# Optimization experiments

Hardware: AMD Instinct MI355X
Metric: run time of the kernel (lower is better)

## Reference

```python
import jax, jax.numpy as jnp
import numpy as np

B, T, H = 1, 2048, 2048
HEADS, DH = 16, 128  # head_dim = H // HEADS
K = 50               # block size
NEG = -1e9


def setup_inputs() -> dict:
    key = jax.random.key(0)
    ks = jax.random.split(key, 6)
    x = jax.random.normal(ks[0], (B, T, H), jnp.float32)
    mask = jnp.ones((B, T), jnp.float32)
    bias = jax.random.normal(ks[1], (B, HEADS, T, T), jnp.float32) * 0.02
    s = 1.0 / np.sqrt(H)
    Wq = jax.random.normal(ks[2], (H, HEADS, DH), jnp.float32) * s
    Wk = jax.random.normal(ks[3], (H, HEADS, DH), jnp.float32) * s
    Wv = jax.random.normal(ks[4], (H, HEADS, DH), jnp.float32) * s
    Wo = jax.random.normal(ks[5], (HEADS, DH, H), jnp.float32) * (1.0 / np.sqrt(H))
    return {"x_BxTxH": x, "mask_BxT": mask, "attention_bias_BxHxTxT": bias,
            "Wq": Wq, "Wk": Wk, "Wv": Wv, "Wo": Wo}


def _local_self_attention(x, mask, bias, Wq, Wk, Wv, Wo):
    b, t, h = x.shape
    extra = K - t % K          # module always pads (pads a full block if t % K == 0)
    p = t + extra
    n = p // K
    # pad + block the inputs: [b, n, K, h]
    xb = jnp.pad(x, ((0, 0), (0, extra), (0, 0))).reshape(b, n, K, h)
    # pad mask with -1e9 (as in the module), block, build pairwise mask via multiply
    mb = jnp.pad(mask, ((0, 0), (0, extra)), constant_values=NEG).reshape(b, n, K)
    pair = mb[..., :, None] * mb[..., None, :]              # [b, n, K, K]
    mask_bias = jnp.where(pair > 0, 0.0, NEG)[:, :, None]   # [b, n, 1, K, K] (broadcast heads)
    # pad attention bias and extract block-diagonal: [b, n, heads, K, K]
    bp = jnp.pad(bias, ((0, 0), (0, 0), (0, extra), (0, extra)))
    nb = bp.reshape(b, HEADS, n, K, n, K)
    idx = jnp.arange(n)
    blk_bias = nb[:, :, idx, :, idx, :]          # [n, b, heads, K, K]
    blk_bias = jnp.transpose(blk_bias, (1, 0, 2, 3, 4))  # [b, n, heads, K, K]
    # per-block multi-head attention (no qkv bias, query scaled by head_dim**-0.5)
    q = jnp.einsum('bnkh,hef->bnkef', xb, Wq) * (DH ** -0.5)
    k = jnp.einsum('bnkh,hef->bnkef', xb, Wk)
    v = jnp.einsum('bnkh,hef->bnkef', xb, Wv)
    logits = jnp.einsum('bnqef,bnkef->bneqk', q, k) + blk_bias + mask_bias
    attn = jax.nn.softmax(logits, axis=-1)
    out = jnp.einsum('bneqk,bnkef->bnqef', attn, v)
    out = jnp.einsum('bnqef,efh->bnqh', out, Wo).reshape(b, p, h)
    return out[:, :t, :]


def reference(x_BxTxH, mask_BxT, attention_bias_BxHxTxT, Wq, Wk, Wv, Wo):
    return _local_self_attention(x_BxTxH, mask_BxT, attention_bias_BxHxTxT, Wq, Wk, Wv, Wo)
```

## Files before the change

### kernel.cpp

```cpp
#include <hip/hip_runtime.h>
#include <hip/hip_bf16.h>

typedef _Float16 f16x8 __attribute__((ext_vector_type(8)));
typedef float f32x4 __attribute__((ext_vector_type(4)));

#define T_DIM 2048
#define H_DIM 2048
#define N_HEADS 16
#define DH 128
#define KBLK 50
#define NBLK 41
#define NEGV (-1.0e9f)
#define QSCALE 0.08838834764831845f

__device__ __forceinline__ void gl_lds16(const void* g, void* l) {
    __builtin_amdgcn_global_load_lds(
        (const __attribute__((address_space(1))) void*)g,
        (__attribute__((address_space(3))) void*)l, 16, 0, 0);
}

__global__ __launch_bounds__(256) void prep_kernel(const float* __restrict__ x,
                                                   const float* __restrict__ Wq,
                                                   const float* __restrict__ Wk,
                                                   const float* __restrict__ Wv,
                                                   const float* __restrict__ Wo,
                                                   _Float16* __restrict__ xb,
                                                   _Float16* __restrict__ WT,
                                                   _Float16* __restrict__ WoT) {
    __shared__ float tile[32][33];
    int z = blockIdx.z;
    int tx = threadIdx.x, ty = threadIdx.y;
    if (z == 4) {
        if (blockIdx.y >= 32) return;
        int flat = blockIdx.y * 64 + blockIdx.x;
        int i = (flat * 256 + ty * 32 + tx) * 8;
        float4 a = *(const float4*)&x[i];
        float4 b = *(const float4*)&x[i + 4];
        f16x8 o = {(_Float16)a.x, (_Float16)a.y, (_Float16)a.z, (_Float16)a.w,
                   (_Float16)b.x, (_Float16)b.y, (_Float16)b.z, (_Float16)b.w};
        *(f16x8*)&xb[i] = o;
        return;
    }
    const float* src = (z == 0) ? Wq : (z == 1) ? Wk : (z == 2) ? Wv : Wo;
    _Float16* dst = (z == 3) ? WoT : (WT + (size_t)z * T_DIM * H_DIM);
    int bx = blockIdx.x * 32, by = blockIdx.y * 32;
#pragma unroll
    for (int i = 0; i < 4; i++)
        tile[ty + i * 8][tx] = src[(size_t)(by + ty + i * 8) * H_DIM + bx + tx];
    __syncthreads();
#pragma unroll
    for (int i = 0; i < 4; i++)
        dst[(size_t)(bx + ty + i * 8) * H_DIM + by + tx] = (_Float16)tile[tx][ty + i * 8];
}

__global__ __launch_bounds__(512, 2) void qkv192_kernel(const _Float16* __restrict__ A,
                                                        const _Float16* __restrict__ BT,
                                                        _Float16* __restrict__ qkv) {
    const int K = 2048, NT = 32;
    __shared__ _Float16 smem[57344];
    _Float16* sA0 = smem;
    _Float16* sA1 = smem + 16384;
    _Float16* sB0 = smem + 32768;
    _Float16* sB1 = smem + 45056;

    int tid = threadIdx.x;
    int lane = tid & 63, wave = tid >> 6;
    int wm = wave >> 2, wn = wave & 3;
    int cb = lane & 15, hi = lane >> 4;

    int bid = blockIdx.x;
    int swz = (bid & 7) * 32 + (bid >> 3);
    int by = swz >> 5, bx = swz & 31;
    int bm = by * 256, bn = bx * 192;

    f32x4 acc[8][3];
#pragma unroll
    for (int m = 0; m < 8; m++)
#pragma unroll
        for (int n = 0; n < 3; n++) acc[m][n] = (f32x4){0.f, 0.f, 0.f, 0.f};

    int rp = tid >> 3, cc = tid & 7;
    int scol = ((cc ^ (rp & 7)) << 3);

    auto stageA = [&](int t, int u) {
        int buf = t & 1;
        gl_lds16(A + (size_t)(bm + u * 64 + rp) * K + (t << 6) + scol,
                 (buf ? sA1 : sA0) + u * 4096 + tid * 8);
    };
    auto stageB = [&](int t, int u) {
        int buf = t & 1;
        gl_lds16(BT + (size_t)(bn + u * 64 + rp) * K + (t << 6) + scol,
                 (buf ? sB1 : sB0) + u * 4096 + tid * 8);
    };

    f16x8 a_lo[4][2], a_hi[4][2], b01[2][2], b2[2];

    stageA(0, 0); stageA(0, 1); stageA(0, 2); stageA(0, 3);
    stageB(0, 0); stageB(0, 1); stageB(0, 2);
    stageA(1, 0); stageA(1, 1); stageA(1, 2); stageA(1, 3);
    asm volatile("s_waitcnt vmcnt(4)" ::: "memory");
    __builtin_amdgcn_s_barrier();

    for (int t = 0; t < NT; t++) {
        int buf = t & 1;
        const char* bA = (const char*)(buf ? sA1 : sA0);
        const char* bB = (const char*)(buf ? sB1 : sB0);
#pragma unroll
        for (int mf = 0; mf < 4; mf++) {
            int ra = wm * 128 + mf * 16 + cb;
#pragma unroll
            for (int ks = 0; ks < 2; ks++)
                a_lo[mf][ks] = *(const f16x8*)(bA + (ra << 7) +
                                               ((ks * 64 + hi * 16) ^ ((ra & 7) << 4)));
        }
#pragma unroll
        for (int nf = 0; nf < 2; nf++) {
            int rb = wn * 48 + nf * 16 + cb;
#pragma unroll
            for (int ks = 0; ks < 2; ks++)
                b01[nf][ks] = *(const f16x8*)(bB + (rb << 7) +
                                              ((ks * 64 + hi * 16) ^ ((rb & 7) << 4)));
        }
        if (t + 1 < NT) { stageB(t + 1, 0); stageB(t + 1, 1); }
        __builtin_amdgcn_s_barrier();
        asm volatile("s_waitcnt lgkmcnt(0)" ::: "memory");
        __builtin_amdgcn_s_setprio(1);
#pragma unroll
        for (int mf = 0; mf < 4; mf++)
#pragma unroll
            for (int nf = 0; nf < 2; nf++)
#pragma unroll
                for (int ks = 0; ks < 2; ks++)
                    acc[mf][nf] = __builtin_amdgcn_mfma_f32_16x16x32_f16(a_lo[mf][ks], b01[nf][ks], acc[mf][nf], 0, 0, 0);
        __builtin_amdgcn_s_setprio(0);
        __builtin_amdgcn_s_barrier();

#pragma unroll
        for (int mf = 0; mf < 4; mf++) {
            int ra = wm * 128 + 64 + mf * 16 + cb;
#pragma unroll
            for (int ks = 0; ks < 2; ks++)
                a_hi[mf][ks] = *(const f16x8*)(bA + (ra << 7) +
                                               ((ks * 64 + hi * 16) ^ ((ra & 7) << 4)));
        }
        {
            int rb = wn * 48 + 32 + cb;
#pragma unroll
            for (int ks = 0; ks < 2; ks++)
                b2[ks] = *(const f16x8*)(bB + (rb << 7) +
                                         ((ks * 64 + hi * 16) ^ ((rb & 7) << 4)));
        }
        if (t + 1 < NT) stageB(t + 1, 2);
        __builtin_amdgcn_s_barrier();
        asm volatile("s_waitcnt lgkmcnt(0)" ::: "memory");
        __builtin_amdgcn_s_setprio(1);
#pragma unroll
        for (int mf = 0; mf < 4; mf++)
#pragma unroll
            for (int ks = 0; ks < 2; ks++)
                acc[4 + mf][2] = __builtin_amdgcn_mfma_f32_16x16x32_f16(a_hi[mf][ks], b2[ks], acc[4 + mf][2], 0, 0, 0);
        __builtin_amdgcn_s_setprio(0);
        __builtin_amdgcn_s_barrier();

        if (t + 2 < NT) { stageA(t + 2, 0); stageA(t + 2, 1); }
        __builtin_amdgcn_s_barrier();
        __builtin_amdgcn_s_setprio(1);
#pragma unroll
        for (int mf = 0; mf < 4; mf++)
#pragma unroll
            for (int ks = 0; ks < 2; ks++)
                acc[mf][2] = __builtin_amdgcn_mfma_f32_16x16x32_f16(a_lo[mf][ks], b2[ks], acc[mf][2], 0, 0, 0);
        __builtin_amdgcn_s_setprio(0);
        __builtin_amdgcn_s_barrier();

        if (t + 2 < NT) { stageA(t + 2, 2); stageA(t + 2, 3); }
        if (t < NT - 2)
            asm volatile("s_waitcnt vmcnt(4)" ::: "memory");
        else if (t == NT - 2)
            asm volatile("s_waitcnt vmcnt(0)" ::: "memory");
        __builtin_amdgcn_s_barrier();
        __builtin_amdgcn_s_setprio(1);
#pragma unroll
        for (int mf = 0; mf < 4; mf++)
#pragma unroll
            for (int nf = 0; nf < 2; nf++)
#pragma unroll
                for (int ks = 0; ks < 2; ks++)
                    acc[4 + mf][nf] = __builtin_amdgcn_mfma_f32_16x16x32_f16(a_hi[mf][ks], b01[nf][ks], acc[4 + mf][nf], 0, 0, 0);
        __builtin_amdgcn_s_setprio(0);
        __builtin_amdgcn_s_barrier();
    }

#pragma unroll
    for (int p = 0; p < 2; p++) {
        if (p) __builtin_amdgcn_s_barrier();
        if (wm == p) {
#pragma unroll
            for (int mf = 0; mf < 8; mf++)
#pragma unroll
                for (int nf = 0; nf < 3; nf++) {
                    int col = wn * 48 + nf * 16 + cb;
                    float sc = ((bn + col) >> 11) == 0 ? QSCALE : 1.0f;
#pragma unroll
                    for (int r = 0; r < 4; r++) {
                        int row = mf * 16 + hi * 4 + r;
                        smem[row * 200 + col] = (_Float16)(acc[mf][nf][r] * sc);
                    }
                }
        }
        __builtin_amdgcn_s_barrier();
#pragma unroll
        for (int it = 0; it < 6; it++) {
            int c = it * 512 + tid;
            int row = c / 24, col8 = c - row * 24;
            int gm = bm + p * 128 + row;
            int gn = bn + col8 * 8;
            int tensor = gn >> 11;
            int ef = gn & 2047;
            int e = ef >> 7, f0 = ef & 127;
            uint4 v = *(const uint4*)&smem[row * 200 + col8 * 8];
            *(uint4*)(qkv + (size_t)tensor * (T_DIM * H_DIM) + (size_t)e * (T_DIM * DH) +
                      (size_t)gm * DH + f0) = v;
        }
    }
}

__global__ __launch_bounds__(512, 2) void oproj_kernel(const _Float16* __restrict__ A,
                                                       const _Float16* __restrict__ BT,
                                                       _Float16* __restrict__ part) {
    const int K = 2048, NT = 8;
    __shared__ _Float16 smem[65536];
    _Float16* sA0 = smem;
    _Float16* sA1 = smem + 16384;
    _Float16* sB0 = smem + 32768;
    _Float16* sB1 = smem + 49152;

    int tid = threadIdx.x;
    int lane = tid & 63, wave = tid >> 6;
    int wm = wave >> 2, wn = wave & 3;
    int cb = lane & 15, hi = lane >> 4;

    int bid = blockIdx.x;
    int s = bid & 3, tile = bid >> 2;
    int by = tile >> 3, bx = tile & 7;
    int bm = by * 256, bn = bx * 256;
    int kbase = s * 512;

    f32x4 acc[8][4];
#pragma unroll
    for (int m = 0; m < 8; m++)
#pragma unroll
        for (int n = 0; n < 4; n++) acc[m][n] = (f32x4){0.f, 0.f, 0.f, 0.f};

    auto stageP = [&](int t, int p) {
        int buf = t & 1, k0 = kbase + (t << 6);
        const _Float16* src = (p < 2) ? A + (size_t)(bm + ((p & 1) << 7)) * K + k0
                                      : BT + (size_t)(bn + ((p & 1) << 7)) * K + k0;
        _Float16* dst = ((p < 2) ? (buf ? sA1 : sA0) : (buf ? sB1 : sB0)) + ((p & 1) << 13);
#pragma unroll
        for (int l = 0; l < 2; l++) {
            int c = l * 512 + tid;
            int rp = c >> 3, cc = c & 7;
            int col = (cc ^ (rp & 7)) << 3;
            gl_lds16(src + (size_t)rp * K + col, dst + c * 8);
        }
    };

    f16x8 a_lo[4][2], a_hi[4][2], b_lo[2][2], b_hi[2][2];

    stageP(0, 0); stageP(0, 1); stageP(0, 2); stageP(0, 3);
    stageP(1, 0); stageP(1, 1);
    asm volatile("s_waitcnt vmcnt(4)" ::: "memory");
    __builtin_amdgcn_s_barrier();

    for (int t = 0; t < NT; t++) {
        int buf = t & 1;
        const char* bA = (const char*)(buf ? sA1 : sA0);
        const char* bB = (const char*)(buf ? sB1 : sB0);
#pragma unroll
        for (int m = 0; m < 4; m++) {
            int ra = wm * 128 + m * 16 + cb;
#pragma unroll
            for (int ks = 0; ks < 2; ks++)
                a_lo[m][ks] = *(const f16x8*)(bA + (ra << 7) +
                                              ((ks * 64 + hi * 16) ^ ((ra & 7) << 4)));
        }
#pragma unroll
        for (int n = 0; n < 2; n++) {
            int rb = wn * 64 + n * 16 + cb;
#pragma unroll
            for (int ks = 0; ks < 2; ks++)
                b_lo[n][ks] = *(const f16x8*)(bB + (rb << 7) +
                                              ((ks * 64 + hi * 16) ^ ((rb & 7) << 4)));
        }
        if (t + 1 < NT) stageP(t + 1, 2);
        __builtin_amdgcn_s_barrier();
        asm volatile("s_waitcnt lgkmcnt(0)" ::: "memory");
        __builtin_amdgcn_s_setprio(1);
#pragma unroll
        for (int m = 0; m < 4; m++)
#pragma unroll
            for (int n = 0; n < 2; n++)
#pragma unroll
                for (int ks = 0; ks < 2; ks++)
                    acc[m][n] = __builtin_amdgcn_mfma_f32_16x16x32_f16(a_lo[m][ks], b_lo[n][ks], acc[m][n], 0, 0, 0);
        __builtin_amdgcn_s_setprio(0);
        __builtin_amdgcn_s_barrier();

#pragma unroll
        for (int m = 0; m < 4; m++) {
            int ra = wm * 128 + 64 + m * 16 + cb;
#pragma unroll
            for (int ks = 0; ks < 2; ks++)
                a_hi[m][ks] = *(const f16x8*)(bA + (ra << 7) +
                                              ((ks * 64 + hi * 16) ^ ((ra & 7) << 4)));
        }
#pragma unroll
        for (int n = 0; n < 2; n++) {
            int rb = wn * 64 + 32 + n * 16 + cb;
#pragma unroll
            for (int ks = 0; ks < 2; ks++)
                b_hi[n][ks] = *(const f16x8*)(bB + (rb << 7) +
                                              ((ks * 64 + hi * 16) ^ ((rb & 7) << 4)));
        }
        if (t + 1 < NT) stageP(t + 1, 3);
        __builtin_amdgcn_s_barrier();
        asm volatile("s_waitcnt lgkmcnt(0)" ::: "memory");
        __builtin_amdgcn_s_setprio(1);
#pragma unroll
        for (int m = 0; m < 4; m++)
#pragma unroll
            for (int n = 0; n < 2; n++)
#pragma unroll
                for (int ks = 0; ks < 2; ks++)
                    acc[4 + m][2 + n] = __builtin_amdgcn_mfma_f32_16x16x32_f16(a_hi[m][ks], b_hi[n][ks], acc[4 + m][2 + n], 0, 0, 0);
        __builtin_amdgcn_s_setprio(0);
        __builtin_amdgcn_s_barrier();

        if (t + 2 < NT) stageP(t + 2, 0);
        __builtin_amdgcn_s_barrier();
        __builtin_amdgcn_s_setprio(1);
#pragma unroll
        for (int m = 0; m < 4; m++)
#pragma unroll
            for (int n = 0; n < 2; n++)
#pragma unroll
                for (int ks = 0; ks < 2; ks++)
                    acc[m][2 + n] = __builtin_amdgcn_mfma_f32_16x16x32_f16(a_lo[m][ks], b_hi[n][ks], acc[m][2 + n], 0, 0, 0);
        __builtin_amdgcn_s_setprio(0);
        __builtin_amdgcn_s_barrier();

        if (t + 2 < NT) stageP(t + 2, 1);
        if (t < NT - 2)
            asm volatile("s_waitcnt vmcnt(4)" ::: "memory");
        else if (t == NT - 2)
            asm volatile("s_waitcnt vmcnt(0)" ::: "memory");
        __builtin_amdgcn_s_barrier();
        __builtin_amdgcn_s_setprio(1);
#pragma unroll
        for (int m = 0; m < 4; m++)
#pragma unroll
            for (int n = 0; n < 2; n++)
#pragma unroll
                for (int ks = 0; ks < 2; ks++)
                    acc[4 + m][n] = __builtin_amdgcn_mfma_f32_16x16x32_f16(a_hi[m][ks], b_lo[n][ks], acc[4 + m][n], 0, 0, 0);
        __builtin_amdgcn_s_setprio(0);
        __builtin_amdgcn_s_barrier();
    }

    _Float16* pb = part + (size_t)s * T_DIM * H_DIM;
#pragma unroll
    for (int p = 0; p < 2; p++) {
        if (p) __builtin_amdgcn_s_barrier();
        if (wm == p) {
#pragma unroll
            for (int m = 0; m < 8; m++)
#pragma unroll
                for (int n = 0; n < 4; n++) {
                    int col = wn * 64 + ((n & 1) * 16) + ((n >> 1) * 32) + cb;
#pragma unroll
                    for (int r = 0; r < 4; r++) {
                        int row = ((m & 3) * 16) + ((m >> 2) * 64) + hi * 4 + r;
                        smem[row * 264 + col] = (_Float16)acc[m][n][r];
                    }
                }
        }
        __builtin_amdgcn_s_barrier();
#pragma unroll
        for (int it = 0; it < 8; it++) {
            int c = it * 512 + tid;
            int row = c >> 5, col8 = c & 31;
            int gm = bm + p * 128 + row;
            int gn = bn + col8 * 8;
            uint4 v = *(const uint4*)&smem[row * 264 + col8 * 8];
            *(uint4*)&pb[(size_t)gm * H_DIM + gn] = v;
        }
    }
}

__global__ __launch_bounds__(256) void reduce4_kernel(const _Float16* __restrict__ part,
                                                      float* __restrict__ out) {
    const size_t S = (size_t)T_DIM * H_DIM;
    int i = (blockIdx.x * 256 + threadIdx.x) * 8;
    f16x8 p0 = *(const f16x8*)&part[i];
    f16x8 p1 = *(const f16x8*)&part[S + i];
    f16x8 p2 = *(const f16x8*)&part[2 * S + i];
    f16x8 p3 = *(const f16x8*)&part[3 * S + i];
#pragma unroll
    for (int j = 0; j < 8; j++)
        out[i + j] = (float)p0[j] + (float)p1[j] + (float)p2[j] + (float)p3[j];
}

__global__ __launch_bounds__(256) void attn_kernel(const _Float16* __restrict__ qkvb,
                                                   const float* __restrict__ bias,
                                                   const float* __restrict__ mask,
                                                   _Float16* __restrict__ aout) {
    int bid = blockIdx.x;
    int n = bid >> 4, e = bid & 15;
    int t0 = n * KBLK;
    int valid = (T_DIM - t0 < KBLK) ? (T_DIM - t0) : KBLK;

    __shared__ _Float16 Qs[64 * 136];
    __shared__ _Float16 Ks[64 * 136];
    __shared__ _Float16 VTs[128 * 72];
    __shared__ _Float16 Ps[64 * 72];
    __shared__ float maskv[64];

    int tid = threadIdx.x;
    int lane = tid & 63, wave = tid >> 6;
    const _Float16* qp = qkvb + (size_t)e * (T_DIM * DH);
    const _Float16* kp = qkvb + (size_t)(T_DIM * H_DIM) + (size_t)e * (T_DIM * DH);
    const _Float16* vp = qkvb + (size_t)2 * (T_DIM * H_DIM) + (size_t)e * (T_DIM * DH);

#pragma unroll
    for (int i = 0; i < 4; i++) {
        int c = tid + i * 256;
        int r = c >> 4, c8 = c & 15;
        uint4 z = {0u, 0u, 0u, 0u};
        uint4 vq = z, vk = z;
        if (r < valid) {
            vq = *(const uint4*)&qp[(size_t)(t0 + r) * DH + c8 * 8];
            vk = *(const uint4*)&kp[(size_t)(t0 + r) * DH + c8 * 8];
        }
        *(uint4*)&Qs[r * 136 + c8 * 8] = vq;
        *(uint4*)&Ks[r * 136 + c8 * 8] = vk;
    }
#pragma unroll
    for (int i = 0; i < 4; i++) {
        int c = tid + i * 256;
        int r = c & 63;
        int f0 = (c >> 6) * 8;
        uint4 v = {0u, 0u, 0u, 0u};
        if (r < valid) v = *(const uint4*)&vp[(size_t)(t0 + r) * DH + f0];
        _Float16 tmp[8];
        *(uint4*)tmp = v;
#pragma unroll
        for (int j = 0; j < 8; j++) VTs[(f0 + j) * 72 + r] = tmp[j];
    }
    if (tid < 64) maskv[tid] = (tid < valid) ? mask[t0 + tid] : NEGV;
    __syncthreads();

    int qr0 = wave * 16;
    int cb = lane & 15, hi = lane >> 4;

    f16x8 aq[4];
#pragma unroll
    for (int ks = 0; ks < 4; ks++)
        aq[ks] = *(const f16x8*)&Qs[(qr0 + cb) * 136 + ks * 32 + hi * 8];
    f32x4 s[4];
#pragma unroll
    for (int kt = 0; kt < 4; kt++) s[kt] = (f32x4){0.f, 0.f, 0.f, 0.f};
#pragma unroll
    for (int kt = 0; kt < 4; kt++)
#pragma unroll
        for (int ks = 0; ks < 4; ks++) {
            f16x8 bk = *(const f16x8*)&Ks[(kt * 16 + cb) * 136 + ks * 32 + hi * 8];
            s[kt] = __builtin_amdgcn_mfma_f32_16x16x32_f16(aq[ks], bk, s[kt], 0, 0, 0);
        }

#pragma unroll
    for (int r = 0; r < 4; r++) {
        int rl = qr0 + hi * 4 + r;
        int qi = t0 + rl;
        float mq = maskv[rl];
        float lg[4];
        float mx = -3.4e38f;
#pragma unroll
        for (int kt = 0; kt < 4; kt++) {
            int cl = kt * 16 + cb, ki = t0 + cl;
            float bg = (qi < T_DIM && ki < T_DIM)
                           ? bias[((size_t)e * T_DIM + qi) * T_DIM + ki] : 0.f;
            float pr = mq * maskv[cl];
            float v = s[kt][r] + bg + (pr > 0.f ? 0.f : NEGV);
            lg[kt] = v;
            mx = fmaxf(mx, v);
        }
#pragma unroll
        for (int off = 8; off; off >>= 1) mx = fmaxf(mx, __shfl_xor(mx, off));
        float sum = 0.f;
#pragma unroll
        for (int kt = 0; kt < 4; kt++) {
            float pe = __expf(lg[kt] - mx);
            lg[kt] = pe;
            sum += pe;
        }
#pragma unroll
        for (int off = 8; off; off >>= 1) sum += __shfl_xor(sum, off);
        float inv = 1.f / sum;
#pragma unroll
        for (int kt = 0; kt < 4; kt++)
            Ps[rl * 72 + kt * 16 + cb] = (_Float16)(lg[kt] * inv);
    }
    __syncthreads();

    f16x8 pa[2];
#pragma unroll
    for (int ks = 0; ks < 2; ks++)
        pa[ks] = *(const f16x8*)&Ps[(qr0 + cb) * 72 + ks * 32 + hi * 8];
#pragma unroll
    for (int ft = 0; ft < 8; ft++) {
        f32x4 o = (f32x4){0.f, 0.f, 0.f, 0.f};
#pragma unroll
        for (int ks = 0; ks < 2; ks++) {
            f16x8 bv = *(const f16x8*)&VTs[(ft * 16 + cb) * 72 + ks * 32 + hi * 8];
            o = __builtin_amdgcn_mfma_f32_16x16x32_f16(pa[ks], bv, o, 0, 0, 0);
        }
#pragma unroll
        for (int r = 0; r < 4; r++) {
            int rl = qr0 + hi * 4 + r;
            if (rl < valid)
                aout[(size_t)(t0 + rl) * H_DIM + e * DH + ft * 16 + cb] = (_Float16)o[r];
        }
    }
}

extern "C" void kernel_launch(void* const* d_in, const int* in_sizes, int n_in,
                              void* d_out, int out_size, void* d_ws, size_t ws_size,
                              hipStream_t stream) {
    const float* x    = (const float*)d_in[0];
    const float* mask = (const float*)d_in[1];
    const float* bias = (const float*)d_in[2];
    const float* Wq   = (const float*)d_in[3];
    const float* Wk   = (const float*)d_in[4];
    const float* Wv   = (const float*)d_in[5];
    const float* Wo   = (const float*)d_in[6];
    float* out = (float*)d_out;

    _Float16* xb   = (_Float16*)d_ws;
    _Float16* WT   = xb + (size_t)T_DIM * H_DIM;
    _Float16* WoT  = WT + (size_t)3 * T_DIM * H_DIM;
    _Float16* qkvb = WoT + (size_t)T_DIM * H_DIM;
    _Float16* aout = qkvb + (size_t)3 * T_DIM * H_DIM;
    _Float16* part = aout + (size_t)T_DIM * H_DIM;

    prep_kernel<<<dim3(64, 64, 5), dim3(32, 8), 0, stream>>>(x, Wq, Wk, Wv, Wo, xb, WT, WoT);

    qkv192_kernel<<<256, 512, 0, stream>>>(xb, WT, qkvb);

    attn_kernel<<<NBLK * N_HEADS, 256, 0, stream>>>(qkvb, bias, mask, aout);

    oproj_kernel<<<256, 512, 0, stream>>>(aout, WoT, part);
    reduce4_kernel<<<(T_DIM * H_DIM) / (256 * 8), 256, 0, stream>>>(part, out);
}
```

Before: 127.0 us.

## Widen prep transpose tiles, remap GEMM block order, stage attention bias in LDS

The weight transpose and convert kernel now uses 64x64 tiles with 4-wide fp16 stores and fewer blocks, and the x conversion handles 16 elements per thread. The QKV and output-projection GEMMs get new block-index mappings that change which tiles run together, which affects L2 reuse. The attention kernel preloads the 50x50 bias block into shared memory with coalesced row loads instead of gathering it per element from global memory inside the softmax. These changes aim to improve memory coalescing and cache locality, at the cost of extra LDS use in attention and possible shifts in GEMM cache behaviour.

```diff
diff --git a/kernel.cpp b/kernel.cpp
--- a/kernel.cpp
+++ b/kernel.cpp
@@ -2,6 +2,7 @@
 #include <hip/hip_bf16.h>
 
 typedef _Float16 f16x8 __attribute__((ext_vector_type(8)));
+typedef _Float16 f16x4 __attribute__((ext_vector_type(4)));
 typedef float f32x4 __attribute__((ext_vector_type(4)));
 
 #define T_DIM 2048
@@ -27,30 +28,41 @@
                                                    _Float16* __restrict__ xb,
                                                    _Float16* __restrict__ WT,
                                                    _Float16* __restrict__ WoT) {
-    __shared__ float tile[32][33];
     int z = blockIdx.z;
     int tx = threadIdx.x, ty = threadIdx.y;
+    int t = ty * 32 + tx;
     if (z == 4) {
-        if (blockIdx.y >= 32) return;
-        int flat = blockIdx.y * 64 + blockIdx.x;
-        int i = (flat * 256 + ty * 32 + tx) * 8;
-        float4 a = *(const float4*)&x[i];
-        float4 b = *(const float4*)&x[i + 4];
-        f16x8 o = {(_Float16)a.x, (_Float16)a.y, (_Float16)a.z, (_Float16)a.w,
-                   (_Float16)b.x, (_Float16)b.y, (_Float16)b.z, (_Float16)b.w};
-        *(f16x8*)&xb[i] = o;
+        int flat = blockIdx.y * 32 + blockIdx.x;
+        int i0 = (flat * 256 + t) * 16;
+#pragma unroll
+        for (int h = 0; h < 2; h++) {
+            float4 a = *(const float4*)&x[i0 + h * 8];
+            float4 b = *(const float4*)&x[i0 + h * 8 + 4];
+            f16x8 o = {(_Float16)a.x, (_Float16)a.y, (_Float16)a.z, (_Float16)a.w,
+                       (_Float16)b.x, (_Float16)b.y, (_Float16)b.z, (_Float16)b.w};
+            *(f16x8*)&xb[i0 + h * 8] = o;
+        }
         return;
     }
+    __shared__ float tile[64][65];
     const float* src = (z == 0) ? Wq : (z == 1) ? Wk : (z == 2) ? Wv : Wo;
     _Float16* dst = (z == 3) ? WoT : (WT + (size_t)z * T_DIM * H_DIM);
-    int bx = blockIdx.x * 32, by = blockIdx.y * 32;
-#pragma unroll
-    for (int i = 0; i < 4; i++)
-        tile[ty + i * 8][tx] = src[(size_t)(by + ty + i * 8) * H_DIM + bx + tx];
+    int bx = blockIdx.x * 64, by = blockIdx.y * 64;
+#pragma unroll
+    for (int i = 0; i < 8; i++) {
+        int row = ty + i * 8;
+        tile[row][tx] = src[(size_t)(by + row) * H_DIM + bx + tx];
+        tile[row][tx + 32] = src[(size_t)(by + row) * H_DIM + bx + tx + 32];
+    }
     __syncthreads();
 #pragma unroll
-    for (int i = 0; i < 4; i++)
-        dst[(size_t)(bx + ty + i * 8) * H_DIM + by + tx] = (_Float16)tile[tx][ty + i * 8];
+    for (int it = 0; it < 4; it++) {
+        int idx = it * 256 + t;
+        int r = idx >> 4, c4 = (idx & 15) * 4;
+        f16x4 v = {(_Float16)tile[c4][r], (_Float16)tile[c4 + 1][r],
+                   (_Float16)tile[c4 + 2][r], (_Float16)tile[c4 + 3][r]};
+        *(f16x4*)&dst[(size_t)(bx + r) * H_DIM + by + c4] = v;
+    }
 }
 
 __global__ __launch_bounds__(512, 2) void qkv192_kernel(const _Float16* __restrict__ A,
@@ -69,8 +81,8 @@
     int cb = lane & 15, hi = lane >> 4;
 
     int bid = blockIdx.x;
-    int swz = (bid & 7) * 32 + (bid >> 3);
-    int by = swz >> 5, bx = swz & 31;
+    int bx = (bid & 7) * 4 + ((bid >> 3) & 3);
+    int by = bid >> 5;
     int bm = by * 256, bn = bx * 192;
 
     f32x4 acc[8][3];
@@ -241,8 +253,9 @@
     int cb = lane & 15, hi = lane >> 4;
 
     int bid = blockIdx.x;
-    int s = bid & 3, tile = bid >> 2;
-    int by = tile >> 3, bx = tile & 7;
+    int bx = bid & 7;
+    int rest = bid >> 3;
+    int by = rest & 7, s = rest >> 3;
     int bm = by * 256, bn = bx * 256;
     int kbase = s * 512;
 
@@ -424,6 +437,7 @@
     __shared__ _Float16 Ks[64 * 136];
     __shared__ _Float16 VTs[128 * 72];
     __shared__ _Float16 Ps[64 * 72];
+    __shared__ float Bs[50 * 64];
     __shared__ float maskv[64];
 
     int tid = threadIdx.x;
@@ -457,6 +471,20 @@
 #pragma unroll
         for (int j = 0; j < 8; j++) VTs[(f0 + j) * 72 + r] = tmp[j];
     }
+    {
+        const float* bp = bias + ((size_t)e * T_DIM + t0) * T_DIM + t0;
+        int klim = T_DIM - t0;
+        if (klim > KBLK) klim = KBLK;
+#pragma unroll
+        for (int i = 0; i < 13; i++) {
+            int idx = i * 256 + tid;
+            int r = idx >> 6, c = idx & 63;
+            if (r < KBLK) {
+                float v = (r < valid && c < klim) ? bp[(size_t)r * T_DIM + c] : 0.f;
+                Bs[r * 64 + c] = v;
+            }
+        }
+    }
     if (tid < 64) maskv[tid] = (tid < valid) ? mask[t0 + tid] : NEGV;
     __syncthreads();
 
@@ -481,15 +509,13 @@
 #pragma unroll
     for (int r = 0; r < 4; r++) {
         int rl = qr0 + hi * 4 + r;
-        int qi = t0 + rl;
         float mq = maskv[rl];
         float lg[4];
         float mx = -3.4e38f;
 #pragma unroll
         for (int kt = 0; kt < 4; kt++) {
-            int cl = kt * 16 + cb, ki = t0 + cl;
-            float bg = (qi < T_DIM && ki < T_DIM)
-                           ? bias[((size_t)e * T_DIM + qi) * T_DIM + ki] : 0.f;
+            int cl = kt * 16 + cb;
+            float bg = (rl < KBLK && cl < KBLK) ? Bs[rl * 64 + cl] : 0.f;
             float pr = mq * maskv[cl];
             float v = s[kt][r] + bg + (pr > 0.f ? 0.f : NEGV);
             lg[kt] = v;
@@ -553,7 +579,7 @@
     _Float16* aout = qkvb + (size_t)3 * T_DIM * H_DIM;
     _Float16* part = aout + (size_t)T_DIM * H_DIM;
 
-    prep_kernel<<<dim3(64, 64, 5), dim3(32, 8), 0, stream>>>(x, Wq, Wk, Wv, Wo, xb, WT, WoT);
+    prep_kernel<<<dim3(32, 32, 5), dim3(32, 8), 0, stream>>>(x, Wq, Wk, Wv, Wo, xb, WT, WoT);
 
     qkv192_kernel<<<256, 512, 0, stream>>>(xb, WT, qkvb);
 
```

Measured after the change: 131.5 us. +3.5%, slower.
